# Optimization experiments

Measured on AMD Instinct MI355X. Metric: run time of the kernel, lower is better.

## Reference

```python
import jax, jax.numpy as jnp
import numpy as np

FEAT_STRIDE = 8
SCALES = (4.0, 8.0, 16.0)
RATIOS = (0.5, 1.0, 2.0)
A = len(SCALES) * len(RATIOS)          # 9 anchors per location
PRE_NMS = 2048
POST_NMS = 300
NMS_THRESH = 0.7


def _gen_base_anchors():
    # cube anchors at scale*stride, ratio applied to depth; boxes (x1,y1,z1,x2,y2,z2)
    base = float(FEAT_STRIDE)
    ctr = (base - 1.0) / 2.0
    boxes = []
    for r in RATIOS:
        for s in SCALES:
            w = h = base * s
            d = base * s * r
            boxes.append([ctr - 0.5 * (w - 1), ctr - 0.5 * (h - 1), ctr - 0.5 * (d - 1),
                          ctr + 0.5 * (w - 1), ctr + 0.5 * (h - 1), ctr + 0.5 * (d - 1)])
    return jnp.asarray(boxes, jnp.float32)  # [A,6]


def _all_anchors(D, H, W):
    sz = jnp.arange(D, dtype=jnp.float32) * FEAT_STRIDE
    sy = jnp.arange(H, dtype=jnp.float32) * FEAT_STRIDE
    sx = jnp.arange(W, dtype=jnp.float32) * FEAT_STRIDE
    zz, yy, xx = jnp.meshgrid(sz, sy, sx, indexing='ij')  # order (d,h,w) matches score layout
    shifts = jnp.stack([xx, yy, zz, xx, yy, zz], -1).reshape(-1, 6)  # [K,6]
    return (shifts[:, None, :] + _gen_base_anchors()[None]).reshape(-1, 6)  # [K*A,6]


def _apply_deltas(anchors, deltas):
    w = anchors[:, 3] - anchors[:, 0] + 1.0
    h = anchors[:, 4] - anchors[:, 1] + 1.0
    d = anchors[:, 5] - anchors[:, 2] + 1.0
    cx = anchors[:, 0] + 0.5 * w
    cy = anchors[:, 1] + 0.5 * h
    cz = anchors[:, 2] + 0.5 * d
    dx, dy, dz, dw, dh, dd = [deltas[:, i] for i in range(6)]
    pcx = dx * w + cx; pcy = dy * h + cy; pcz = dz * d + cz
    pw = jnp.exp(dw) * w; ph = jnp.exp(dh) * h; pd = jnp.exp(dd) * d
    return jnp.stack([pcx - 0.5 * pw, pcy - 0.5 * ph, pcz - 0.5 * pd,
                      pcx + 0.5 * pw, pcy + 0.5 * ph, pcz + 0.5 * pd], -1)


def _clip_boxes(boxes, iminfo):  # iminfo = [D_im, H_im, W_im]
    lo = jnp.zeros((6,), boxes.dtype)
    hi = jnp.stack([iminfo[2], iminfo[1], iminfo[0], iminfo[2], iminfo[1], iminfo[0]]) - 1.0
    return jnp.clip(boxes, lo[None, :], hi[None, :])


def _pairwise_iou3d(b):  # b: [N,6]
    lo = jnp.maximum(b[:, None, :3], b[None, :, :3])          # [N,N,3]
    hi = jnp.minimum(b[:, None, 3:], b[None, :, 3:])
    inter = jnp.prod(jnp.clip(hi - lo + 1.0, 0.0), axis=-1)   # [N,N]
    vol = jnp.prod(b[:, 3:] - b[:, :3] + 1.0, axis=-1)        # [N]
    return inter / (vol[:, None] + vol[None, :] - inter)


def _nms_keep(iou):
    N = iou.shape[0]
    idx = jnp.arange(N)
    def body(i, keep):
        sup = (iou[i] > NMS_THRESH) & keep[i] & (idx > i)
        return keep & ~sup
    return jax.lax.fori_loop(0, N, body, jnp.ones((N,), bool))


def _propose_one(scores, deltas, anchors, iminfo):
    boxes = _clip_boxes(_apply_deltas(anchors, deltas), iminfo)  # [KA,6]
    _, order = jax.lax.top_k(scores, PRE_NMS)
    b = boxes[order]                                             # [PRE,6], score-sorted desc
    keep = _nms_keep(_pairwise_iou3d(b))
    key = jnp.where(keep, jnp.arange(PRE_NMS), PRE_NMS)
    sel = jnp.argsort(key)[:POST_NMS]                            # first POST_NMS kept, in score order
    valid = (key[sel] < PRE_NMS).astype(b.dtype)
    return b[sel] * valid[:, None]                               # zero-padded rows if < POST_NMS kept


def _forward(base_feat, im_info, W_conv, b_conv, W_cls, b_cls, W_bbox, b_bbox):
    B, C, D, H, W = base_feat.shape
    x = jax.lax.conv_general_dilated(
        base_feat, W_conv, (1, 1, 1), ((1, 1), (1, 1), (1, 1)),
        dimension_numbers=('NCDHW', 'OIDHW', 'NCDHW'))
    x = jax.nn.relu(x + b_conv[None, :, None, None, None])       # [B,512,D,H,W]
    cls = jnp.einsum('bcdhw,oc->bodhw', x, W_cls) + b_cls[None, :, None, None, None]
    prob = jax.nn.softmax(cls.reshape(B, 2, A, D, H, W), axis=1)  # reshape(x,2) + softmax(dim=1)
    fg = prob[:, 1]                                               # [B,A,D,H,W]
    scores = jnp.transpose(fg, (0, 2, 3, 4, 1)).reshape(B, -1)    # [B, K*A], order (d,h,w,a)
    bb = jnp.einsum('bcdhw,oc->bodhw', x, W_bbox) + b_bbox[None, :, None, None, None]
    deltas = jnp.transpose(bb.reshape(B, A, 6, D, H, W), (0, 3, 4, 5, 1, 2)).reshape(B, -1, 6)
    anchors = _all_anchors(D, H, W)
    rois6 = jax.vmap(lambda s, d, im: _propose_one(s, d, anchors, im))(scores, deltas, im_info)
    bidx = jnp.broadcast_to(jnp.arange(B, dtype=rois6.dtype)[:, None, None], (B, POST_NMS, 1))
    return jnp.concatenate([bidx, rois6], -1)                     # [B, POST_NMS, 7]


def setup_inputs() -> dict:
    key = jax.random.key(0)
    ks = jax.random.split(key, 4)
    B, din, D, H, W = 2, 128, 8, 32, 32
    base_feat = jax.random.normal(ks[0], (B, din, D, H, W), jnp.float32)
    im_info = jnp.asarray([[64.0, 256.0, 256.0]] * B, jnp.float32)  # (D_im, H_im, W_im)
    gt_boxes = jnp.zeros((B, 20, 7), jnp.float32)
    num_boxes = jnp.zeros((B,), jnp.int64)
    W_conv = jax.random.normal(ks[1], (512, din, 3, 3, 3), jnp.float32) * 0.02
    b_conv = jnp.zeros((512,), jnp.float32)
    W_cls = jax.random.normal(ks[2], (2 * A, 512), jnp.float32) * 0.01
    b_cls = jnp.zeros((2 * A,), jnp.float32)
    W_bbox = jax.random.normal(ks[3], (6 * A, 512), jnp.float32) * 0.01
    b_bbox = jnp.zeros((6 * A,), jnp.float32)
    return {"base_feat": base_feat, "im_info": im_info, "gt_boxes": gt_boxes,
            "num_boxes": num_boxes, "W_conv": W_conv, "b_conv": b_conv,
            "W_cls": W_cls, "b_cls": b_cls, "W_bbox": W_bbox, "b_bbox": b_bbox}


def reference(base_feat, im_info, gt_boxes, num_boxes, W_conv, b_conv, W_cls, b_cls, W_bbox, b_bbox):
    # Eval-mode RPN forward: losses are 0 in the original; gt_boxes/num_boxes unused.
    rois = _forward(base_feat, im_info, W_conv, b_conv, W_cls, b_cls, W_bbox, b_bbox)
    return rois
```

## Files before the change

kernel.cpp:

```cpp
#include <hip/hip_runtime.h>
#include <stdint.h>

#define BATCH 2
#define CIN 128
#define COUT 512
#define DD 8
#define PSPAT 8192
#define NA 9
#define NANCH 73728
#define PRE 2048
#define POST 300
#define CAP 4096
#define NMS_TH 0.7f

typedef unsigned short u16;
typedef _Float16 f16x8 __attribute__((ext_vector_type(8)));
typedef float f32x16 __attribute__((ext_vector_type(16)));
typedef unsigned int uint32x4 __attribute__((ext_vector_type(4)));

constexpr size_t OFF_WT   = 0;
constexpr size_t OFF_WHT  = 7077888;
constexpr size_t OFF_X    = 7241728;
constexpr size_t OFF_SC   = 40796160;
constexpr size_t OFF_BX   = 41385984;
constexpr size_t OFF_SB   = 44957696;
constexpr size_t OFF_MK   = 45056000;
constexpr size_t OFF_HIST = 16;
constexpr size_t OFF_CAND = 524304;
constexpr size_t OFF_XH   = 46104576;
constexpr size_t OFF_XL   = 50298880;
constexpr size_t WS_NEED_FAST = 54493184;

#define NT_WT   (27 * 128 * 512)
#define NT_WHT  (512 * 80)
__global__ void k_wtrans(const float* __restrict__ Wc, u16* __restrict__ Wg,
                         const float* __restrict__ Wcls, const float* __restrict__ Wbb,
                         float* __restrict__ Wht) {
    int e = blockIdx.x * blockDim.x + threadIdx.x;
    if (e < NT_WT) {
        const int k    = e & 63;
        const int n    = (e >> 6) & 127;
        const int half = (e >> 13) & 1;
        const int rest = e >> 14;
        const int co = (rest / 27) * 128 + n;
        const int ci = half * 64 + k;
        const int tp = rest % 27;
        const float v = Wc[(co * 128 + ci) * 27 + tp] * 1024.f;
        const _Float16 h = (_Float16)v;
        const _Float16 l = (_Float16)(v - (float)h);
        char* rb = (char*)Wg + (((size_t)(rest * 2 + half)) << 15) + n * 256;
        const int hcol = (k >> 3) ^ (n & 15);
        const int lcol = ((k >> 3) | 8) ^ (n & 15);
        const int kb = (k & 7) << 1;
        *(u16*)(rb + (hcol << 4) + kb) = __builtin_bit_cast(unsigned short, h);
        *(u16*)(rb + (lcol << 4) + kb) = __builtin_bit_cast(unsigned short, l);
        return;
    }
    e -= NT_WT;
    if (e >= NT_WHT) return;
    int q = e % 80;
    int c = e / 80;
    int og = q / 10, k = q % 10;
    int o = og * 9 + k;
    float v = 0.f;
    if (k < 9) v = (o < 18) ? Wcls[o * 512 + c] : Wbb[(o - 18) * 512 + c];
    Wht[e] = v;
}

__global__ __launch_bounds__(256) void k_split(const float* __restrict__ in,
                                               u16* __restrict__ xh, u16* __restrict__ xl) {
    __shared__ float t[128][33];
    const int blk = blockIdx.x;
    const int b = blk >> 8, d = (blk >> 5) & 7, h = blk & 31;
    const int tid = threadIdx.x;
    const float* src = in + ((size_t)b << 20) + d * 1024 + h * 32;
    #pragma unroll
    for (int i = 0; i < 16; ++i) {
        const int e = tid + i * 256;
        const int ci = e >> 5, w = e & 31;
        t[ci][w] = src[(size_t)ci * 8192 + w];
    }
    __syncthreads();
    const size_t ob = (size_t)((b * 8 + d) * 32 + h) * 4096;
    #pragma unroll
    for (int i = 0; i < 16; ++i) {
        const int e = tid + i * 256;
        const int w = e >> 7, ci = e & 127;
        const float v = t[ci][w] * 1024.f;
        const _Float16 hh = (_Float16)v;
        const _Float16 ll = (_Float16)(v - (float)hh);
        xh[ob + w * 128 + ci] = __builtin_bit_cast(unsigned short, hh);
        xl[ob + w * 128 + ci] = __builtin_bit_cast(unsigned short, ll);
    }
}

#define MFMA(A, B, C) __builtin_amdgcn_mfma_f32_32x32x16_f16((A), (B), (C), 0, 0, 0)
#define Z16 {0.f,0.f,0.f,0.f,0.f,0.f,0.f,0.f,0.f,0.f,0.f,0.f,0.f,0.f,0.f,0.f}

#define WISSUE(S, BUF) { \
    const int tap_ = t0 + ((S) >> 1); \
    const char* gw_ = WgB + (((size_t)((nt * 27 + tap_) * 2 + ((S) & 1))) << 15) \
                    + (wv << 13) + ln16; \
    char* lb_ = smem + ((BUF) << 15) + (wv << 13); \
    _Pragma("unroll") \
    for (int j_ = 0; j_ < 8; ++j_) \
        __builtin_amdgcn_global_load_lds( \
            (const __attribute__((address_space(1))) void*)(gw_ + (j_ << 10)), \
            (__attribute__((address_space(3))) void*)(lb_ + (j_ << 10)), 16, 0, 0); }

#define KKSTEP(KK, BH0, BL0, BH1, BL1) { \
    const int ch_ = ((((KK) << 1) + cq) ^ rsw) << 4; \
    const int cl_ = (((((KK) << 1) + cq) | 8) ^ rsw) << 4; \
    const char* r0_ = wb_ + (rm0 << 8); \
    const char* r1_ = wb_ + (rm1 << 8); \
    const f16x8 wh0 = *(const f16x8*)(r0_ + ch_); \
    const f16x8 wl0 = *(const f16x8*)(r0_ + cl_); \
    const f16x8 wh1 = *(const f16x8*)(r1_ + ch_); \
    const f16x8 wl1 = *(const f16x8*)(r1_ + cl_); \
    acc00 = MFMA(wh0, BH0, acc00); acc00 = MFMA(wh0, BL0, acc00); acc00 = MFMA(wl0, BH0, acc00); \
    acc01 = MFMA(wh0, BH1, acc01); acc01 = MFMA(wh0, BL1, acc01); acc01 = MFMA(wl0, BH1, acc01); \
    acc10 = MFMA(wh1, BH0, acc10); acc10 = MFMA(wh1, BL0, acc10); acc10 = MFMA(wl1, BH0, acc10); \
    acc11 = MFMA(wh1, BH1, acc11); acc11 = MFMA(wh1, BL1, acc11); acc11 = MFMA(wl1, BH1, acc11); }

#define EPI(ACC, MI, NI) { \
    const int coB_ = co0 + (wm << 6) + ((MI) << 5) + hl4; \
    const int pt_  = p0 + (wn << 6) + ((NI) << 5) + l31; \
    _Pragma("unroll") \
    for (int g_ = 0; g_ < 4; ++g_) { \
        _Pragma("unroll") \
        for (int q_ = 0; q_ < 4; ++q_) { \
            const int co_ = coB_ + (g_ << 3) + q_; \
            const float v_ = ACC[g_ * 4 + q_] * 9.5367431640625e-07f + bconv[co_]; \
            x[((size_t)((b << 9) + co_) << 13) + pt_] = fmaxf(v_, 0.f); \
        } } }

#define FLD(N, KK, BH, BL) { \
    const int h2_ = hb_ + (N); \
    const bool ok_ = okw_ && ((unsigned)h2_ < 32u); \
    const size_t ix_ = sbase_ + ((size_t)((h2_ & 31) << 5) << 7); \
    const f16x8 vh_ = *(const f16x8*)(xh + ix_ + ((KK) << 4)); \
    const f16x8 vl_ = *(const f16x8*)(xl + ix_ + ((KK) << 4)); \
    BH = ok_ ? vh_ : fz8; \
    BL = ok_ ? vl_ : fz8; }

#define ALOADF(S, P) { \
    const int tap_ = t0 + ((S) >> 1); \
    const int kd_ = tap_ / 9, kh_ = (tap_ / 3) % 3, kw_ = tap_ % 3; \
    const int id_ = d0 + kd_ - 1; \
    const int w2_ = l31 + kw_ - 1; \
    const bool okw_ = (unsigned)w2_ < 32u; \
    const int hb_ = h0 + (wn << 1) + kh_ - 1; \
    const int cio_ = (((S) & 1) << 6) + (cq << 3); \
    const size_t sbase_ = (((size_t)((b << 3) + id_)) << 17) + ((w2_ & 31) << 7) + cio_; \
    FLD(0, 0, P##h00, P##l00) FLD(0, 1, P##h01, P##l01) \
    FLD(0, 2, P##h02, P##l02) FLD(0, 3, P##h03, P##l03) \
    FLD(1, 0, P##h10, P##l10) FLD(1, 1, P##h11, P##l11) \
    FLD(1, 2, P##h12, P##l12) FLD(1, 3, P##h13, P##l13) }

#define COMPUTEF(BUF, P) { \
    const char* wb_ = smem + ((BUF) << 15); \
    KKSTEP(0, P##h00, P##l00, P##h10, P##l10) \
    KKSTEP(1, P##h01, P##l01, P##h11, P##l11) \
    KKSTEP(2, P##h02, P##l02, P##h12, P##l12) \
    KKSTEP(3, P##h03, P##l03, P##h13, P##l13) }

__global__ __launch_bounds__(256, 2) void k_conv_f(const u16* __restrict__ xh,
                                                   const u16* __restrict__ xl,
                                                   const u16* __restrict__ Wg,
                                                   const float* __restrict__ bconv,
                                                   float* __restrict__ x) {
    __shared__ __align__(16) char smem[65536];
    const int tid  = threadIdx.x;
    const int bx   = blockIdx.x;
    const int nt   = blockIdx.y;
    const int b    = blockIdx.z;
    const int p0   = bx << 7;
    const int d0   = bx >> 3;
    const int h0   = (bx & 7) << 2;
    const int co0  = nt << 7;

    const int lane = tid & 63;
    const int wv   = tid >> 6;
    const int wm   = wv & 1;
    const int wn   = wv >> 1;
    const int l31  = lane & 31;
    const int cq   = lane >> 5;
    const int hl4  = cq << 2;
    const int rsw  = l31 & 15;
    const int rm0  = (wm << 6) + l31;
    const int rm1  = rm0 + 32;
    const int ln16 = lane << 4;

    const int t0   = (d0 == 0) ? 9 : 0;
    const int nTap = 27 - (((d0 == 0) || (d0 == 7)) ? 9 : 0);
    const int NS   = nTap * 2;

    const char* WgB = (const char*)Wg;
    const f16x8 fz8 = {(_Float16)0.f, (_Float16)0.f, (_Float16)0.f, (_Float16)0.f,
                       (_Float16)0.f, (_Float16)0.f, (_Float16)0.f, (_Float16)0.f};

    f16x8 Ah00, Al00, Ah01, Al01, Ah02, Al02, Ah03, Al03,
          Ah10, Al10, Ah11, Al11, Ah12, Al12, Ah13, Al13;
    f16x8 Bh00, Bl00, Bh01, Bl01, Bh02, Bl02, Bh03, Bl03,
          Bh10, Bl10, Bh11, Bl11, Bh12, Bl12, Bh13, Bl13;
    f32x16 acc00 = Z16, acc01 = Z16, acc10 = Z16, acc11 = Z16;

    WISSUE(0, 0)
    ALOADF(0, A)
    __syncthreads();

    for (int s = 0; s < NS; s += 2) {
        WISSUE(s + 1, 1)
        ALOADF(s + 1, B)
        __builtin_amdgcn_sched_barrier(0);
        COMPUTEF(0, A)
        __syncthreads();
        if (s + 2 < NS) { WISSUE(s + 2, 0) ALOADF(s + 2, A) }
        __builtin_amdgcn_sched_barrier(0);
        COMPUTEF(1, B)
        __syncthreads();
    }

    EPI(acc00, 0, 0)
    EPI(acc01, 0, 1)
    EPI(acc10, 1, 0)
    EPI(acc11, 1, 1)
}

#define PK2(YA, YB, UH, UL) { \
    const float sa_ = (YA) * 1024.f, sb_ = (YB) * 1024.f; \
    const _Float16 ha_ = (_Float16)sa_, hb_ = (_Float16)sb_; \
    const _Float16 la_ = (_Float16)(sa_ - (float)ha_); \
    const _Float16 lb_ = (_Float16)(sb_ - (float)hb_); \
    UH = (unsigned)__builtin_bit_cast(unsigned short, ha_) | \
         ((unsigned)__builtin_bit_cast(unsigned short, hb_) << 16); \
    UL = (unsigned)__builtin_bit_cast(unsigned short, la_) | \
         ((unsigned)__builtin_bit_cast(unsigned short, lb_) << 16); }

#define BLDI(N, KK) { \
    const int h2_ = hb_ + (N); \
    const bool ok_ = okw_ && ((unsigned)h2_ < 32u); \
    const float* ap_ = in + (((size_t)(cb0_ + ((KK) << 4))) << 13) + spo_ + (h2_ << 5); \
    y[N][KK][0] = ok_ ? ap_[0]     : 0.f; \
    y[N][KK][1] = ok_ ? ap_[8192]  : 0.f; \
    y[N][KK][2] = ok_ ? ap_[16384] : 0.f; \
    y[N][KK][3] = ok_ ? ap_[24576] : 0.f; \
    y[N][KK][4] = ok_ ? ap_[32768] : 0.f; \
    y[N][KK][5] = ok_ ? ap_[40960] : 0.f; \
    y[N][KK][6] = ok_ ? ap_[49152] : 0.f; \
    y[N][KK][7] = ok_ ? ap_[57344] : 0.f; }

#define ALOADISS(S) { \
    const int tap_ = t0 + ((S) >> 1); \
    const int kd_ = tap_ / 9, kh_ = (tap_ / 3) % 3, kw_ = tap_ % 3; \
    const int id_ = d0 + kd_ - 1; \
    const int w2_ = l31 + kw_ - 1; \
    const bool okw_ = (unsigned)w2_ < 32u; \
    const int hb_ = h0 + (wn << 1) + kh_ - 1; \
    const int cb0_ = b * CIN + (((S) & 1) << 6) + (cq << 3); \
    const long long spo_ = ((long long)id_ << 10) + w2_; \
    BLDI(0, 0) BLDI(0, 1) BLDI(0, 2) BLDI(0, 3) \
    BLDI(1, 0) BLDI(1, 1) BLDI(1, 2) BLDI(1, 3) }

#define CVTFRAG(N, KK, BH, BL) { \
    unsigned uh0_, uh1_, uh2_, uh3_, ul0_, ul1_, ul2_, ul3_; \
    PK2(y[N][KK][0], y[N][KK][1], uh0_, ul0_) \
    PK2(y[N][KK][2], y[N][KK][3], uh1_, ul1_) \
    PK2(y[N][KK][4], y[N][KK][5], uh2_, ul2_) \
    PK2(y[N][KK][6], y[N][KK][7], uh3_, ul3_) \
    { uint32x4 th_ = {uh0_, uh1_, uh2_, uh3_}; BH = __builtin_bit_cast(f16x8, th_); } \
    { uint32x4 tl_ = {ul0_, ul1_, ul2_, ul3_}; BL = __builtin_bit_cast(f16x8, tl_); } }

#define CVTALL() { \
    CVTFRAG(0, 0, bh00, bl00) CVTFRAG(0, 1, bh01, bl01) \
    CVTFRAG(0, 2, bh02, bl02) CVTFRAG(0, 3, bh03, bl03) \
    CVTFRAG(1, 0, bh10, bl10) CVTFRAG(1, 1, bh11, bl11) \
    CVTFRAG(1, 2, bh12, bl12) CVTFRAG(1, 3, bh13, bl13) }

#define COMPUTE(BUF) { \
    const char* wb_ = smem + ((BUF) << 15); \
    KKSTEP(0, bh00, bl00, bh10, bl10) \
    KKSTEP(1, bh01, bl01, bh11, bl11) \
    KKSTEP(2, bh02, bl02, bh12, bl12) \
    KKSTEP(3, bh03, bl03, bh13, bl13) }

__global__ __launch_bounds__(256, 2) void k_conv(const float* __restrict__ in,
                                                 const u16* __restrict__ Wg,
                                                 const float* __restrict__ bconv,
                                                 float* __restrict__ x) {
    __shared__ __align__(16) char smem[65536];
    const int tid  = threadIdx.x;
    const int bx   = blockIdx.x;
    const int nt   = blockIdx.y;
    const int b    = blockIdx.z;
    const int p0   = bx << 7;
    const int d0   = bx >> 3;
    const int h0   = (bx & 7) << 2;
    const int co0  = nt << 7;

    const int lane = tid & 63;
    const int wv   = tid >> 6;
    const int wm   = wv & 1;
    const int wn   = wv >> 1;
    const int l31  = lane & 31;
    const int cq   = lane >> 5;
    const int hl4  = cq << 2;
    const int rsw  = l31 & 15;
    const int rm0  = (wm << 6) + l31;
    const int rm1  = rm0 + 32;
    const int ln16 = lane << 4;

    const int t0   = (d0 == 0) ? 9 : 0;
    const int nTap = 27 - (((d0 == 0) || (d0 == 7)) ? 9 : 0);
    const int NS   = nTap * 2;

    const char* WgB = (const char*)Wg;

    float y[2][4][8];
    f16x8 bh00, bh01, bh02, bh03, bh10, bh11, bh12, bh13;
    f16x8 bl00, bl01, bl02, bl03, bl10, bl11, bl12, bl13;
    f32x16 acc00 = Z16, acc01 = Z16, acc10 = Z16, acc11 = Z16;

    WISSUE(0, 0)
    ALOADISS(0)
    __syncthreads();

    for (int s = 0; s < NS; ++s) {
        if (s + 1 < NS) { WISSUE(s + 1, (s + 1) & 1) }
        CVTALL()
        __builtin_amdgcn_sched_barrier(0);
        if (s + 1 < NS) { ALOADISS(s + 1) }
        __builtin_amdgcn_sched_barrier(0);
        COMPUTE(s & 1)
        __syncthreads();
    }

    EPI(acc00, 0, 0)
    EPI(acc01, 0, 1)
    EPI(acc10, 1, 0)
    EPI(acc11, 1, 1)
}

__global__ __launch_bounds__(256) void k_heads(const float* __restrict__ x,
                                               const float* __restrict__ Wht,
                                               const float* __restrict__ bcls,
                                               const float* __restrict__ bbb,
                                               const float* __restrict__ iminfo,
                                               float* __restrict__ scores,
                                               float* __restrict__ boxes,
                                               unsigned int* __restrict__ hist) {
    __shared__ __align__(16) float smx[4096];
    __shared__ __align__(16) float Whs[2560];
    __shared__ __align__(16) float ex[10240];
    const int tid = threadIdx.x;
    const int p0  = blockIdx.x * 128;
    const int b   = blockIdx.y;
    const int pl  = tid & 31;
    const int og  = tid >> 5;

    float acc[4][9] = {};

    for (int cc = 0; cc < 512; cc += 32) {
        __syncthreads();
        #pragma unroll
        for (int i = 0; i < 4; ++i) {
            int e4 = tid + i * 256;
            int ch = e4 >> 5;
            int pt4 = (e4 & 31) * 4;
            *(float4*)&smx[ch * 128 + pt4] =
                *(const float4*)&x[((size_t)(b * COUT + cc + ch) << 13) + p0 + pt4];
        }
        #pragma unroll
        for (int i = 0; i < 10; ++i) {
            int e = tid + i * 256;
            Whs[e] = Wht[cc * 80 + e];
        }
        __syncthreads();
        for (int kk = 0; kk < 32; ++kk) {
            float4 a4 = *(const float4*)&smx[kk * 128 + pl * 4];
            const float* wp = &Whs[kk * 80 + og * 10];
            float2 w0 = *(const float2*)(wp);
            float2 w1 = *(const float2*)(wp + 2);
            float2 w2 = *(const float2*)(wp + 4);
            float2 w3 = *(const float2*)(wp + 6);
            float  w8 = wp[8];
            float wv[9] = {w0.x, w0.y, w1.x, w1.y, w2.x, w2.y, w3.x, w3.y, w8};
            #pragma unroll
            for (int k = 0; k < 9; ++k) {
                float wk = wv[k];
                acc[0][k] += a4.x * wk;
                acc[1][k] += a4.y * wk;
                acc[2][k] += a4.z * wk;
                acc[3][k] += a4.w * wk;
            }
        }
    }

    __syncthreads();
    #pragma unroll
    for (int pi = 0; pi < 4; ++pi)
        #pragma unroll
        for (int k = 0; k < 9; ++k)
            ex[(pl * 4 + pi) * 80 + og * 10 + k] = acc[pi][k];
    __syncthreads();

    if (tid < 128) {
        const int p = p0 + tid;
        float v[72];
        #pragma unroll
        for (int og2 = 0; og2 < 8; ++og2)
            #pragma unroll
            for (int k = 0; k < 9; ++k)
                v[og2 * 9 + k] = ex[tid * 80 + og2 * 10 + k];

        const float im0 = iminfo[b * 3 + 0], im1 = iminfo[b * 3 + 1], im2 = iminfo[b * 3 + 2];
        const float hix = im2 - 1.f, hiy = im1 - 1.f, hiz = im0 - 1.f;
        const int d = p >> 10, h = (p >> 5) & 31, w = p & 31;
        const float sx = w * 8.f, sy = h * 8.f, sz = d * 8.f;

        #pragma unroll 1
        for (int a = 0; a < 9; ++a) {
            float c0 = v[a] + bcls[a];
            float c1 = v[9 + a] + bcls[9 + a];
            float m  = fmaxf(c0, c1);
            float e0 = expf(c0 - m), e1 = expf(c1 - m);
            float sc = e1 / (e0 + e1);
            scores[b * NANCH + p * 9 + a] = sc;
            atomicAdd(&hist[b * 65536 + (__float_as_uint(sc) >> 16)], 1u);

            float aw = (float)(32 << (a % 3));
            float ad = aw * 0.5f * (float)(1 << (a / 3));
            float ax1 = sx + 3.5f - 0.5f * (aw - 1.f);
            float ax2 = sx + 3.5f + 0.5f * (aw - 1.f);
            float ay1 = sy + 3.5f - 0.5f * (aw - 1.f);
            float ay2 = sy + 3.5f + 0.5f * (aw - 1.f);
            float az1 = sz + 3.5f - 0.5f * (ad - 1.f);
            float az2 = sz + 3.5f + 0.5f * (ad - 1.f);
            float ww_ = ax2 - ax1 + 1.f, hh_ = ay2 - ay1 + 1.f, dd_ = az2 - az1 + 1.f;
            float cx = ax1 + 0.5f * ww_, cy = ay1 + 0.5f * hh_, cz = az1 + 0.5f * dd_;

            const float* dv = &v[18 + a * 6];
            float dx = dv[0] + bbb[a * 6 + 0];
            float dy = dv[1] + bbb[a * 6 + 1];
            float dz = dv[2] + bbb[a * 6 + 2];
            float dw = dv[3] + bbb[a * 6 + 3];
            float dh = dv[4] + bbb[a * 6 + 4];
            float dd2 = dv[5] + bbb[a * 6 + 5];
            float pcx = dx * ww_ + cx, pcy = dy * hh_ + cy, pcz = dz * dd_ + cz;
            float pw = expf(dw) * ww_, ph = expf(dh) * hh_, pd = expf(dd2) * dd_;
            float x1 = fminf(fmaxf(pcx - 0.5f * pw, 0.f), hix);
            float y1 = fminf(fmaxf(pcy - 0.5f * ph, 0.f), hiy);
            float z1 = fminf(fmaxf(pcz - 0.5f * pd, 0.f), hiz);
            float x2 = fminf(fmaxf(pcx + 0.5f * pw, 0.f), hix);
            float y2 = fminf(fmaxf(pcy + 0.5f * ph, 0.f), hiy);
            float z2 = fminf(fmaxf(pcz + 0.5f * pd, 0.f), hiz);
            float* bp = &boxes[(size_t)(b * NANCH + p * 9 + a) * 6];
            bp[0] = x1; bp[1] = y1; bp[2] = z1; bp[3] = x2; bp[4] = y2; bp[5] = z2;
        }
    }
}

__global__ __launch_bounds__(1024) void k_cutcompact(const float* __restrict__ scores,
                                                     const unsigned int* __restrict__ hist,
                                                     unsigned long long* __restrict__ cand) {
    __shared__ unsigned int cs[1024], scan[1024];
    __shared__ unsigned int sh_cut, sh_pos;
    const int b = blockIdx.x, tid = threadIdx.x;
    const unsigned int* h = hist + b * 65536;
    unsigned int s = 0;
    for (int i = 0; i < 64; ++i) s += h[tid * 64 + i];
    cs[tid] = s; scan[tid] = s;
    if (tid == 0) sh_pos = 0;
    __syncthreads();
    for (int d = 1; d < 1024; d <<= 1) {
        unsigned int v = scan[tid];
        unsigned int add = (tid + d < 1024) ? scan[tid + d] : 0u;
        __syncthreads();
        scan[tid] = v + add;
        __syncthreads();
    }
    unsigned int above = (tid + 1 < 1024) ? scan[tid + 1] : 0u;
    if (above < PRE && above + cs[tid] >= PRE) {
        unsigned int cum = above;
        for (int x = tid * 64 + 63; x >= tid * 64; --x) {
            cum += h[x];
            if (cum >= PRE) { sh_cut = (unsigned int)x; break; }
        }
    }
    __syncthreads();
    const unsigned int cut = sh_cut;
    const float* sc = scores + b * NANCH;
    for (int i = tid; i < NANCH; i += 1024) {
        unsigned int u = __float_as_uint(sc[i]);
        if ((u >> 16) >= cut) {
            unsigned int pos = atomicAdd(&sh_pos, 1u);
            if (pos < CAP) cand[b * CAP + pos] = ((unsigned long long)(~u) << 32) | (unsigned)i;
        }
    }
    __syncthreads();
    const unsigned int cnt = (sh_pos < CAP) ? sh_pos : CAP;
    for (int i = (int)cnt + tid; i < CAP; i += 1024)
        cand[b * CAP + i] = ~0ull;
}

__global__ __launch_bounds__(1024) void k_sort2(const unsigned long long* __restrict__ cand,
                                                const float* __restrict__ boxes,
                                                float* __restrict__ sboxes) {
    __shared__ unsigned long long sk[CAP];
    const int b = blockIdx.x, tid = threadIdx.x;
    for (int i = tid; i < CAP; i += 1024) sk[i] = cand[b * CAP + i];
    __syncthreads();
    for (int k = 2; k <= CAP; k <<= 1) {
        for (int j = k >> 1; j > 0; j >>= 1) {
            #pragma unroll 1
            for (int i = tid; i < CAP; i += 1024) {
                int ixj = i ^ j;
                if (ixj > i) {
                    unsigned long long va = sk[i], vb = sk[ixj];
                    bool up = ((i & k) == 0);
                    if ((va > vb) == up) { sk[i] = vb; sk[ixj] = va; }
                }
            }
            __syncthreads();
        }
    }
    for (int r = tid; r < PRE; r += 1024) {
        unsigned int n = (unsigned int)(sk[r] & 0xFFFFFFFFull);
        const float* src = &boxes[(size_t)(b * NANCH + (int)n) * 6];
        float* dst = &sboxes[(size_t)(b * PRE + r) * 6];
        #pragma unroll
        for (int c = 0; c < 6; ++c) dst[c] = src[c];
    }
}

__global__ __launch_bounds__(256) void k_mask(const float* __restrict__ sboxes,
                                              unsigned long long* __restrict__ mask) {
    if (blockIdx.y < blockIdx.x) return;
    __shared__ float rb[64 * 6], cb[64 * 6];
    const int i0 = blockIdx.x * 64, j0 = blockIdx.y * 64, b = blockIdx.z;
    const int tid = threadIdx.x;
    for (int e = tid; e < 384; e += 256) {
        rb[e] = sboxes[(size_t)(b * PRE + i0) * 6 + e];
        cb[e] = sboxes[(size_t)(b * PRE + j0) * 6 + e];
    }
    __syncthreads();
    const int wave = tid >> 6, lane = tid & 63;
    const float bx1 = cb[lane * 6 + 0], by1 = cb[lane * 6 + 1], bz1 = cb[lane * 6 + 2];
    const float bx2 = cb[lane * 6 + 3], by2 = cb[lane * 6 + 4], bz2 = cb[lane * 6 + 5];
    const float vb = (bx2 - bx1 + 1.f) * (by2 - by1 + 1.f) * (bz2 - bz1 + 1.f);
    const int j = j0 + lane;
    for (int rr = 0; rr < 16; ++rr) {
        const int il = wave * 16 + rr;
        const int i = i0 + il;
        float ax1 = rb[il * 6 + 0], ay1 = rb[il * 6 + 1], az1 = rb[il * 6 + 2];
        float ax2 = rb[il * 6 + 3], ay2 = rb[il * 6 + 4], az2 = rb[il * 6 + 5];
        float va = (ax2 - ax1 + 1.f) * (ay2 - ay1 + 1.f) * (az2 - az1 + 1.f);
        float ix = fmaxf(fminf(ax2, bx2) - fmaxf(ax1, bx1) + 1.f, 0.f);
        float iy = fmaxf(fminf(ay2, by2) - fmaxf(ay1, by1) + 1.f, 0.f);
        float iz = fmaxf(fminf(az2, bz2) - fmaxf(az1, bz1) + 1.f, 0.f);
        float inter = ix * iy * iz;
        float iou = inter / (va + vb - inter);
        bool bit = (j > i) && (iou > NMS_TH);
        unsigned long long word = __ballot(bit);
        if (lane == 0) mask[(size_t)(b * PRE + i) * 32 + (j0 >> 6)] = word;
    }
}

__global__ __launch_bounds__(64) void k_nms(const unsigned long long* __restrict__ mask,
                                            const float* __restrict__ sboxes,
                                            float* __restrict__ out) {
    const int b = blockIdx.x, lane = threadIdx.x;
    __shared__ int sel[POST];
    unsigned long long keep = ~0ull;
    const int lw = lane & 31;
    const unsigned long long* mrow = mask + (size_t)b * PRE * 32 + lw;
    unsigned long long b0 = mrow[0 * 32], b1 = mrow[1 * 32], b2 = mrow[2 * 32], b3 = mrow[3 * 32];
    unsigned long long b4 = mrow[4 * 32], b5 = mrow[5 * 32], b6 = mrow[6 * 32], b7 = mrow[7 * 32];
    int kcount = 0;

#define NMS_STEP(J, BUF)                                                        \
    {                                                                           \
        int i = i0 + (J);                                                       \
        unsigned long long cur = (lw >= (i >> 6)) ? BUF : 0ull;                 \
        int nr = i0 + 8 + (J);                                                  \
        BUF = (nr < PRE) ? mrow[(size_t)nr * 32] : 0ull;                        \
        unsigned long long kw = __shfl(keep, i >> 6);                           \
        if ((kw >> (i & 63)) & 1ull) {                                          \
            if (lane < 32) keep &= ~cur;                                        \
            if (lane == 0 && kcount < POST) sel[kcount] = i;                    \
            ++kcount;                                                           \
            if (kcount >= POST) goto nms_done;                                  \
        }                                                                       \
    }

    for (int i0 = 0; i0 < PRE; i0 += 8) {
        NMS_STEP(0, b0) NMS_STEP(1, b1) NMS_STEP(2, b2) NMS_STEP(3, b3)
        NMS_STEP(4, b4) NMS_STEP(5, b5) NMS_STEP(6, b6) NMS_STEP(7, b7)
    }
nms_done:
    __syncthreads();
    const int kc = kcount;
    for (int r = lane; r < POST; r += 64) {
        float* op = &out[(size_t)(b * POST + r) * 7];
        op[0] = (float)b;
        if (r < kc) {
            const float* sb = &sboxes[(size_t)(b * PRE + sel[r]) * 6];
            #pragma unroll
            for (int c = 0; c < 6; ++c) op[1 + c] = sb[c];
        } else {
            #pragma unroll
            for (int c = 0; c < 6; ++c) op[1 + c] = 0.f;
        }
    }
#undef NMS_STEP
}

extern "C" void kernel_launch(void* const* d_in, const int* in_sizes, int n_in,
                              void* d_out, int out_size, void* d_ws, size_t ws_size,
                              hipStream_t stream) {
    const float* base_feat = (const float*)d_in[0];
    const float* im_info   = (const float*)d_in[1];
    const float* W_conv    = (const float*)d_in[4];
    const float* b_conv    = (const float*)d_in[5];
    const float* W_cls     = (const float*)d_in[6];
    const float* b_cls     = (const float*)d_in[7];
    const float* W_bbox    = (const float*)d_in[8];
    const float* b_bbox    = (const float*)d_in[9];

    char* ws = (char*)d_ws;
    u16* Wg        = (u16*)(ws + OFF_WT);
    float* Wht     = (float*)(ws + OFF_WHT);
    float* x       = (float*)(ws + OFF_X);
    float* scores  = (float*)(ws + OFF_SC);
    float* boxes   = (float*)(ws + OFF_BX);
    float* sboxes  = (float*)(ws + OFF_SB);
    unsigned long long* mask = (unsigned long long*)(ws + OFF_MK);
    unsigned int* hist = (unsigned int*)(ws + OFF_HIST);
    unsigned long long* cand = (unsigned long long*)(ws + OFF_CAND);
    u16* xh        = (u16*)(ws + OFF_XH);
    u16* xl        = (u16*)(ws + OFF_XL);

    const int NTRANS = NT_WT + NT_WHT;
    k_wtrans<<<(NTRANS + 255) / 256, 256, 0, stream>>>(W_conv, Wg, W_cls, W_bbox, Wht);
    if (ws_size >= WS_NEED_FAST) {
        k_split<<<512, 256, 0, stream>>>(base_feat, xh, xl);
        k_conv_f<<<dim3(64, 4, 2), 256, 0, stream>>>(xh, xl, Wg, b_conv, x);
    } else {
        k_conv<<<dim3(64, 4, 2), 256, 0, stream>>>(base_feat, Wg, b_conv, x);
    }
    hipMemsetAsync(hist, 0, BATCH * 65536 * sizeof(unsigned int), stream);
    k_heads<<<dim3(64, 2), 256, 0, stream>>>(x, Wht, b_cls, b_bbox, im_info, scores, boxes, hist);
    k_cutcompact<<<BATCH, 1024, 0, stream>>>(scores, hist, cand);
    k_sort2<<<BATCH, 1024, 0, stream>>>(cand, boxes, sboxes);
    k_mask<<<dim3(32, 32, 2), 256, 0, stream>>>(sboxes, mask);
    k_nms<<<BATCH, 64, 0, stream>>>(mask, sboxes, (float*)d_out);
}
```

Before: 667.1 us.

## Replace full syncthreads with counted vmcnt waits in conv pipeline

Swaps __syncthreads in the double-buffered implicit-GEMM conv loop for explicit s_waitcnt vmcnt(N) plus raw s_barrier. Only the older batch of global loads (weights to LDS, activations to registers) has to retire before compute, so the next stage's loads stay in flight during the MFMA work. This relies on exact load counts per stage, and if those counts are wrong a race or stale data can result.

```diff
diff --git a/kernel.cpp b/kernel.cpp
--- a/kernel.cpp
+++ b/kernel.cpp
@@ -164,6 +164,12 @@
     KKSTEP(2, P##h02, P##l02, P##h12, P##l12) \
     KKSTEP(3, P##h03, P##l03, P##h13, P##l13) }
 
+#define VMCNT24 asm volatile("s_waitcnt vmcnt(24)" ::: "memory");
+#define VMCNT16 asm volatile("s_waitcnt vmcnt(16)" ::: "memory");
+#define VMCNT0  asm volatile("s_waitcnt vmcnt(0)"  ::: "memory");
+#define SBAR    __builtin_amdgcn_s_barrier();
+#define SCHED0  __builtin_amdgcn_sched_barrier(0);
+
 __global__ __launch_bounds__(256, 2) void k_conv_f(const u16* __restrict__ xh,
                                                    const u16* __restrict__ xl,
                                                    const u16* __restrict__ Wg,
@@ -206,19 +212,34 @@
     f32x16 acc00 = Z16, acc01 = Z16, acc10 = Z16, acc11 = Z16;
 
     WISSUE(0, 0)
+    SCHED0
     ALOADF(0, A)
-    __syncthreads();
+    VMCNT16
+    SBAR
 
     for (int s = 0; s < NS; s += 2) {
         WISSUE(s + 1, 1)
+        SCHED0
         ALOADF(s + 1, B)
-        __builtin_amdgcn_sched_barrier(0);
+        VMCNT24
+        SCHED0
         COMPUTEF(0, A)
-        __syncthreads();
-        if (s + 2 < NS) { WISSUE(s + 2, 0) ALOADF(s + 2, A) }
-        __builtin_amdgcn_sched_barrier(0);
+        VMCNT16
+        SBAR
+        if (s + 2 < NS) {
+            WISSUE(s + 2, 0)
+            SCHED0
+            ALOADF(s + 2, A)
+            VMCNT24
+        } else {
+            VMCNT0
+        }
+        SCHED0
         COMPUTEF(1, B)
-        __syncthreads();
+        if (s + 2 < NS) {
+            VMCNT16
+            SBAR
+        }
     }
 
     EPI(acc00, 0, 0)
```

Result: faster. 642.2 us (-3.7%).
